# Kernel optimization log

Measured on AMD Instinct MI355X. Metric: run time of the kernel, lower is better.

The kernel has to match this reference:

```python
import jax, jax.numpy as jnp
import numpy as np
from jax import lax

DIM = 384
HEADS = 8
DS = 2  # down_scale


def setup_inputs() -> dict:
    key = jax.random.key(0)
    ks = jax.random.split(key, 6)
    d = DIM
    x = jax.random.normal(ks[0], (1, d, 192, 192), jnp.float32)
    w_qkv = jax.random.normal(ks[1], (3 * d, d), jnp.float32) * 0.02   # 1x1 conv dim->3dim
    b_qkv = jnp.zeros((3 * d,), jnp.float32)
    w_dw = jax.random.normal(ks[2], (3 * d, 1, 3, 3), jnp.float32) * 0.1  # depthwise 3x3
    b_dw = jnp.zeros((3 * d,), jnp.float32)
    w_proj = jax.random.normal(ks[3], (d, d), jnp.float32) * 0.02      # 1x1 conv dim->dim
    b_proj = jnp.zeros((d,), jnp.float32)
    temperature = jnp.ones((HEADS, 1, 1), jnp.float32)
    a1 = jnp.array([0.2], jnp.float32)
    a2 = jnp.array([0.2], jnp.float32)
    a3 = jnp.array([0.2], jnp.float32)
    a4 = jnp.array([0.2], jnp.float32)
    return {"x": x, "w_qkv": w_qkv, "b_qkv": b_qkv, "w_dw": w_dw, "b_dw": b_dw,
            "w_proj": w_proj, "b_proj": b_proj, "temperature": temperature,
            "a1": a1, "a2": a2, "a3": a3, "a4": a4}


def _topk_softmax(attn, kk):
    # exact scatter semantics of torch: mask=1 at top-k indices along last dim
    idx = lax.top_k(attn, kk)[1]                                   # [b,h,C,kk]
    mask = jax.nn.one_hot(idx, attn.shape[-1], dtype=attn.dtype).sum(-2)  # [b,h,C,C]
    return jax.nn.softmax(jnp.where(mask > 0, attn, -jnp.inf), axis=-1)


def reference(x, w_qkv, b_qkv, w_dw, b_dw, w_proj, b_proj, temperature, a1, a2, a3, a4):
    b, c, h, w = x.shape
    # 1x1 qkv conv
    qkv = jnp.einsum('bchw,oc->bohw', x, w_qkv) + b_qkv[None, :, None, None]
    # adaptive_max_pool2d to (h//DS, w//DS) == strided max pool since h,w % DS == 0
    hs, ws = h // DS, w // DS
    qkv = qkv.reshape(b, 3 * c, hs, DS, ws, DS).max(axis=(3, 5))
    # 3x3 depthwise conv, padding=1
    qkv = lax.conv_general_dilated(qkv, w_dw, (1, 1), 'SAME',
                                   feature_group_count=3 * c,
                                   dimension_numbers=('NCHW', 'OIHW', 'NCHW'))
    qkv = qkv + b_dw[None, :, None, None]
    q, k, v = jnp.split(qkv, 3, axis=1)
    hw = hs * ws
    C = c // HEADS
    q = q.reshape(b, HEADS, C, hw)
    k = k.reshape(b, HEADS, C, hw)
    v = v.reshape(b, HEADS, C, hw)
    # L2 normalize along spatial dim (F.normalize, eps=1e-12)
    q = q / jnp.clip(jnp.linalg.norm(q, axis=-1, keepdims=True), 1e-12)
    k = k / jnp.clip(jnp.linalg.norm(k, axis=-1, keepdims=True), 1e-12)
    # channel attention: [b,h,C,C]
    attn = jnp.einsum('bhcn,bhdn->bhcd', q, k) * temperature[None]
    out = (_topk_softmax(attn, C // 2) @ v) * a1 \
        + (_topk_softmax(attn, C * 2 // 3) @ v) * a2 \
        + (_topk_softmax(attn, C * 3 // 4) @ v) * a3 \
        + (_topk_softmax(attn, C * 4 // 5) @ v) * a4
    out = out.reshape(b, c, hs, ws)
    out = jax.nn.gelu(out, approximate=False)  # nn.GELU() exact erf form
    # nearest-neighbor upsample back to (h, w) == repeat by DS (exact since h = DS*hs)
    out = jnp.repeat(jnp.repeat(out, DS, axis=2), DS, axis=3)
    out = jnp.einsum('bchw,oc->bohw', out, w_proj) + b_proj[None, :, None, None]
    return out
```

## Files before the change

### kernel.cpp

```cpp
#include <hip/hip_runtime.h>
#include <hip/hip_bf16.h>
#include <math.h>

#define NH    8
#define CPH   48
#define D     384
#define QC    1152
#define HF    192
#define WFULL 192
#define HP    96
#define WP    96
#define NP    9216
#define NF    36864

typedef __attribute__((ext_vector_type(8))) short short8;
typedef __attribute__((ext_vector_type(4))) float f32x4;

__device__ __forceinline__ float gelu_exact(float v) {
    return 0.5f * v * (1.f + erff(v * 0.70710678118654752440f));
}
__device__ __forceinline__ ushort f2bf(float v) {
    __hip_bfloat16 h = __float2bfloat16(v);
    return *reinterpret_cast<ushort*>(&h);
}
__device__ __forceinline__ float bf2f(ushort u) {
    __hip_bfloat16 h = *reinterpret_cast<__hip_bfloat16*>(&u);
    return __bfloat162float(h);
}

__global__ __launch_bounds__(256) void k_prep_w(
    const float* __restrict__ w, ushort* __restrict__ wh, ushort* __restrict__ wl, int n) {
    int i = blockIdx.x * 256 + threadIdx.x;
    if (i < n) {
        float v = w[i];
        ushort h = f2bf(v);
        wh[i] = h;
        wl[i] = f2bf(v - bf2f(h));
    }
}

__global__ __launch_bounds__(256) void k_prep(
    const float* __restrict__ wq, ushort* __restrict__ wh, ushort* __restrict__ wl,
    const float* __restrict__ x, ushort* __restrict__ xh, ushort* __restrict__ xl) {
    __shared__ float xf[64][132];
    const int tid = threadIdx.x;
    if (blockIdx.x < 1728) {
        int i = blockIdx.x * 256 + tid;
        float v = wq[i];
        ushort h = f2bf(v);
        wh[i] = h;
        wl[i] = f2bf(v - bf2f(h));
        return;
    }
    const int e  = blockIdx.x - 1728;
    const int xt = e % 288, kt = e / 288;
    const int kk = kt * 64;
    const int q0 = xt * 32;
    const int py = q0 / 96, px0 = q0 - py * 96;
    const int y0 = 2 * py, xcol0 = 2 * px0;
    const float* xb = x + (size_t)kk * NF + (size_t)y0 * WFULL + xcol0;
#pragma unroll
    for (int it = 0; it < 8; it++) {
        int li = tid + 256 * it;
        int ch = li >> 5, r = (li >> 4) & 1, c4 = (li & 15) * 4;
        float4 v = *(const float4*)&xb[(size_t)ch * NF + r * WFULL + c4];
        *(float4*)&xf[ch][r * 64 + c4] = v;
    }
    __syncthreads();
    const int row = tid >> 1, half = tid & 1;
    const int r = (row >> 1) & 1;
    const int col = (row >> 2) * 2 + (row & 1);
    const int src = r * 64 + col;
    const size_t np = (size_t)xt * 128 + row;
    ushort hbuf[32], lbuf[32];
#pragma unroll
    for (int j = 0; j < 32; j++) {
        float v = xf[half * 32 + j][src];
        ushort h = f2bf(v);
        hbuf[j] = h;
        lbuf[j] = f2bf(v - bf2f(h));
    }
    ushort* dh = xh + np * D + kk + half * 32;
    ushort* dl = xl + np * D + kk + half * 32;
#pragma unroll
    for (int j = 0; j < 4; j++) {
        *(short8*)&dh[j * 8] = *(const short8*)&hbuf[j * 8];
        *(short8*)&dl[j * 8] = *(const short8*)&lbuf[j * 8];
    }
}

__global__ __launch_bounds__(512) void k_qkv_mfma(
    const ushort* __restrict__ xh, const ushort* __restrict__ xl,
    const ushort* __restrict__ wh, const ushort* __restrict__ wl,
    const float* __restrict__ bq, float* __restrict__ pooled) {
    __shared__ ushort lds[4][4096];
    const int tid = threadIdx.x;
    const int lane = tid & 63, wid = tid >> 6;
    const int wm = wid >> 2, wn = wid & 3;

    const int d   = blockIdx.x;
    const int xcd = d & 7;
    const int idx = d >> 3;
    const int by  = xcd * 36 + idx / 9;
    const int bx  = idx % 9;
    const int n0 = bx * 128;
    const int m0 = by * 128;

    const ushort* srcs[4];
    srcs[0] = xh + (size_t)m0 * D;
    srcs[1] = xl + (size_t)m0 * D;
    srcs[2] = wh + (size_t)n0 * D;
    srcs[3] = wl + (size_t)n0 * D;

    f32x4 acc[4][2];
#pragma unroll
    for (int i = 0; i < 4; i++)
#pragma unroll
        for (int j = 0; j < 2; j++) acc[i][j] = (f32x4){0.f, 0.f, 0.f, 0.f};

    int a_off[4], b_off[2];
#pragma unroll
    for (int f = 0; f < 4; f++) {
        int ra = wm * 64 + f * 16 + (lane & 15);
        a_off[f] = ra * 64 + ((((lane >> 4) ^ ((ra >> 1) & 3)) & 3) << 4);
    }
#pragma unroll
    for (int f = 0; f < 2; f++) {
        int rb = wn * 32 + f * 16 + (lane & 15);
        b_off[f] = rb * 64 + ((((lane >> 4) ^ ((rb >> 1) & 3)) & 3) << 4);
    }

    auto STAGE = [&](int kk) {
#pragma unroll
        for (int i = 0; i < 4; i++) {
            const int row = wid * 16 + (lane >> 2);
            const int scol = (((lane & 3) ^ ((row >> 1) & 3)) & 3) << 4;
            const ushort* src = srcs[i] + (size_t)row * D + kk + (scol >> 1);
            __builtin_amdgcn_global_load_lds(
                (const __attribute__((address_space(1))) void*)src,
                (__attribute__((address_space(3))) void*)&lds[i][wid * 512],
                16, 0, 0);
        }
    };

    for (int t = 0; t < 12; ++t) {
        STAGE(t * 32);
        asm volatile("s_waitcnt vmcnt(0)" ::: "memory");
        __builtin_amdgcn_s_barrier();

        const char* bA0 = (const char*)&lds[0][0];
        const char* bA1 = (const char*)&lds[1][0];
        const char* bB0 = (const char*)&lds[2][0];
        const char* bB1 = (const char*)&lds[3][0];
        short8 A[2][4], B[2][2];
#pragma unroll
        for (int f = 0; f < 4; f++) {
            A[0][f] = *(const short8*)(bA0 + a_off[f]);
            A[1][f] = *(const short8*)(bA1 + a_off[f]);
        }
#pragma unroll
        for (int f = 0; f < 2; f++) {
            B[0][f] = *(const short8*)(bB0 + b_off[f]);
            B[1][f] = *(const short8*)(bB1 + b_off[f]);
        }
        __builtin_amdgcn_s_setprio(1);
#pragma unroll
        for (int fm = 0; fm < 4; fm++)
#pragma unroll
            for (int fn = 0; fn < 2; fn++) {
                acc[fm][fn] = __builtin_amdgcn_mfma_f32_16x16x32_bf16(A[0][fm], B[0][fn], acc[fm][fn], 0, 0, 0);
                acc[fm][fn] = __builtin_amdgcn_mfma_f32_16x16x32_bf16(A[0][fm], B[1][fn], acc[fm][fn], 0, 0, 0);
                acc[fm][fn] = __builtin_amdgcn_mfma_f32_16x16x32_bf16(A[1][fm], B[0][fn], acc[fm][fn], 0, 0, 0);
            }
        __builtin_amdgcn_s_setprio(0);
        if (t < 11) __builtin_amdgcn_s_barrier();
    }

    const int p_base = by * 32 + wm * 16 + (lane >> 4);
#pragma unroll
    for (int fn = 0; fn < 2; fn++) {
        const int o = n0 + wn * 32 + fn * 16 + (lane & 15);
        const float b = bq[o];
#pragma unroll
        for (int fm = 0; fm < 4; fm++) {
            f32x4 v = acc[fm][fn];
            float mx = fmaxf(fmaxf(v.x, v.y), fmaxf(v.z, v.w)) + b;
            pooled[(size_t)o * NP + p_base + fm * 4] = mx;
        }
    }
}

__global__ __launch_bounds__(256) void k_dwconv(
    const float* __restrict__ pooled, const float* __restrict__ wd,
    const float* __restrict__ bd, float* __restrict__ out) {
    int gid = blockIdx.x * 256 + threadIdx.x;
    int xq = gid % 24, t = gid / 24;
    int y = t % 96, ch = t / 96;
    const float* src = pooled + (size_t)ch * NP;
    const float* w = wd + ch * 9;
    const int x0 = xq * 4;
    float b = bd[ch];
    float o0 = b, o1 = b, o2 = b, o3 = b;
#pragma unroll
    for (int dy = 0; dy < 3; dy++) {
        int yy = y + dy - 1;
        if (yy < 0 || yy >= HP) continue;
        const float* r = src + yy * WP;
        float4 c = *(const float4*)&r[x0];
        float lm = (x0 > 0) ? r[x0 - 1] : 0.f;
        float rm = (x0 < 92) ? r[x0 + 4] : 0.f;
        float w0 = w[dy * 3], w1 = w[dy * 3 + 1], w2 = w[dy * 3 + 2];
        o0 += w0 * lm  + w1 * c.x + w2 * c.y;
        o1 += w0 * c.x + w1 * c.y + w2 * c.z;
        o2 += w0 * c.y + w1 * c.z + w2 * c.w;
        o3 += w0 * c.z + w1 * c.w + w2 * rm;
    }
    *(float4*)&out[(size_t)ch * NP + y * WP + x0] = make_float4(o0, o1, o2, o3);
}

__global__ __launch_bounds__(256) void k_attn_part(
    const float* __restrict__ qkv, float* __restrict__ Spart,
    float* __restrict__ qnpart, float* __restrict__ knpart) {
    __shared__ float qs[48][196], ks[48][196];
    const int tid = threadIdx.x;
    const int p = blockIdx.x, h = blockIdx.y;
    const int n0 = p * 192;
    const float* qb = qkv + (size_t)(h * CPH) * NP + n0;
    const float* kb = qkv + (size_t)(D + h * CPH) * NP + n0;
#pragma unroll
    for (int it = 0; it < 9; it++) {
        int li = tid + 256 * it;
        int row = li / 48, c4 = (li - row * 48) * 4;
        *(float4*)&qs[row][c4] = *(const float4*)&qb[(size_t)row * NP + c4];
        *(float4*)&ks[row][c4] = *(const float4*)&kb[(size_t)row * NP + c4];
    }
    __syncthreads();
    const int tr = (tid >> 4) * 3, tc = (tid & 15) * 3;
    float acc[3][3] = {};
    for (int n = 0; n < 192; n++) {
        float qv[3], kv[3];
#pragma unroll
        for (int i = 0; i < 3; i++) qv[i] = qs[tr + i][n];
#pragma unroll
        for (int j = 0; j < 3; j++) kv[j] = ks[tc + j][n];
#pragma unroll
        for (int i = 0; i < 3; i++)
#pragma unroll
            for (int j = 0; j < 3; j++) acc[i][j] += qv[i] * kv[j];
    }
    float* Sp = Spart + (size_t)(p * NH + h) * 2304;
#pragma unroll
    for (int i = 0; i < 3; i++)
#pragma unroll
        for (int j = 0; j < 3; j++)
            Sp[(tr + i) * CPH + tc + j] = acc[i][j];
    if (tid < 48) {
        float s = 0.f;
        for (int n = 0; n < 192; n++) s += qs[tid][n] * qs[tid][n];
        qnpart[(p * NH + h) * CPH + tid] = s;
    } else if (tid >= 64 && tid < 112) {
        int t2 = tid - 64;
        float s = 0.f;
        for (int n = 0; n < 192; n++) s += ks[t2][n] * ks[t2][n];
        knpart[(p * NH + h) * CPH + t2] = s;
    }
}

__global__ __launch_bounds__(256) void k_softmax(
    const float* __restrict__ Spart, const float* __restrict__ qnpart,
    const float* __restrict__ knpart, const float* __restrict__ temp,
    const float* __restrict__ a1, const float* __restrict__ a2,
    const float* __restrict__ a3, const float* __restrict__ a4,
    float* __restrict__ Wc) {
    __shared__ float rowbuf[4][64];
    int lane = threadIdx.x & 63;
    int w = threadIdx.x >> 6;
    int row = blockIdx.x * 4 + w;
    int h = row / CPH, c = row % CPH;
    float a = -INFINITY;
    if (lane < CPH) {
        float s = 0.f, q2 = 0.f, k2 = 0.f;
        for (int p = 0; p < 48; p++) {
            int base = (p * NH + h);
            s  += Spart[(size_t)base * 2304 + c * CPH + lane];
            q2 += qnpart[base * CPH + c];
            k2 += knpart[base * CPH + lane];
        }
        float nq = fmaxf(sqrtf(fmaxf(q2, 0.f)), 1e-12f);
        float nk = fmaxf(sqrtf(fmaxf(k2, 0.f)), 1e-12f);
        a = s / (nq * nk) * temp[h];
    }
    rowbuf[w][lane] = a;
    __syncthreads();
    int rank = 0;
    float m = -INFINITY;
    for (int j = 0; j < CPH; j++) {
        float vj = rowbuf[w][j];
        m = fmaxf(m, vj);
        rank += (vj > a || (vj == a && j < lane)) ? 1 : 0;
    }
    float e = (lane < CPH) ? expf(a - m) : 0.f;
    float4 p;
    p.x = (rank < 24) ? e : 0.f;
    p.y = (rank < 32) ? e : 0.f;
    p.z = (rank < 36) ? e : 0.f;
    p.w = (rank < 38) ? e : 0.f;
#pragma unroll
    for (int off = 32; off > 0; off >>= 1) {
        p.x += __shfl_xor(p.x, off);
        p.y += __shfl_xor(p.y, off);
        p.z += __shfl_xor(p.z, off);
        p.w += __shfl_xor(p.w, off);
    }
    if (lane < CPH) {
        float wv = 0.f;
        if (rank < 24) wv += a1[0] / p.x;
        if (rank < 32) wv += a2[0] / p.y;
        if (rank < 36) wv += a3[0] / p.z;
        if (rank < 38) wv += a4[0] / p.w;
        Wc[(h * CPH + c) * CPH + lane] = e * wv;
    }
}

__global__ __launch_bounds__(256) void k_av_gelu(
    const float* __restrict__ qkv, const float* __restrict__ Wc,
    ushort* __restrict__ o96h, ushort* __restrict__ o96l) {
    __shared__ float Ws[3][48][16];
    __shared__ float vs[48][256];
    const int tid = threadIdx.x;
    const int b = blockIdx.x;
    const int h = b / 36;
    const int pc = b - h * 36;
    const int px0 = pc * 256;
    for (int li = tid; li < 2304; li += 256) {
        int t3 = li / 768, r = li - t3 * 768;
        int dd = r >> 4, cc = r & 15;
        Ws[t3][dd][cc] = Wc[(h * CPH + t3 * 16 + cc) * CPH + dd];
    }
    const float* vb = qkv + (size_t)(2 * D + h * CPH) * NP + px0;
#pragma unroll
    for (int it = 0; it < 12; it++) {
        int li = tid + 256 * it;
        int dd = li >> 6, c4 = (li & 63) * 4;
        *(float4*)&vs[dd][c4] = *(const float4*)&vb[(size_t)dd * NP + c4];
    }
    __syncthreads();
    for (int t3 = 0; t3 < 3; t3++) {
        float acc[16] = {};
#pragma unroll 4
        for (int dd = 0; dd < 48; dd++) {
            float vv = vs[dd][tid];
            float4 w0 = *(const float4*)&Ws[t3][dd][0];
            float4 w1 = *(const float4*)&Ws[t3][dd][4];
            float4 w2 = *(const float4*)&Ws[t3][dd][8];
            float4 w3 = *(const float4*)&Ws[t3][dd][12];
            acc[0]  += w0.x * vv; acc[1]  += w0.y * vv; acc[2]  += w0.z * vv; acc[3]  += w0.w * vv;
            acc[4]  += w1.x * vv; acc[5]  += w1.y * vv; acc[6]  += w1.z * vv; acc[7]  += w1.w * vv;
            acc[8]  += w2.x * vv; acc[9]  += w2.y * vv; acc[10] += w2.z * vv; acc[11] += w2.w * vv;
            acc[12] += w3.x * vv; acc[13] += w3.y * vv; acc[14] += w3.z * vv; acc[15] += w3.w * vv;
        }
        short8 hv0, hv1, lv0, lv1;
#pragma unroll
        for (int j = 0; j < 8; j++) {
            float g = gelu_exact(acc[j]);
            ushort hu = f2bf(g);
            hv0[j] = (short)hu; lv0[j] = (short)f2bf(g - bf2f(hu));
            float g2 = gelu_exact(acc[8 + j]);
            ushort hu2 = f2bf(g2);
            hv1[j] = (short)hu2; lv1[j] = (short)f2bf(g2 - bf2f(hu2));
        }
        size_t base = (size_t)(px0 + tid) * D + h * CPH + t3 * 16;
        *(short8*)&o96h[base] = hv0;
        *(short8*)&o96h[base + 8] = hv1;
        *(short8*)&o96l[base] = lv0;
        *(short8*)&o96l[base + 8] = lv1;
    }
}

__global__ __launch_bounds__(256) void k_proj_mfma(
    const ushort* __restrict__ wph, const ushort* __restrict__ wpl,
    const ushort* __restrict__ o96h, const ushort* __restrict__ o96l,
    const float* __restrict__ bp, float* __restrict__ out) {
    __shared__ ushort lds[2][4][4096];
    const int tid = threadIdx.x;
    const int lane = tid & 63, wid = tid >> 6;
    const int wm = wid >> 1, wn = wid & 1;

    const int d   = blockIdx.x;
    const int xcd = d & 7;
    const int idx = d >> 3;
    const int nt  = xcd * 9 + idx / 3;
    const int ot  = idx % 3;
    const int o0 = ot * 128;
    const int n0 = nt * 128;

    const ushort* srcs[4];
    srcs[0] = wph + (size_t)o0 * D;
    srcs[1] = wpl + (size_t)o0 * D;
    srcs[2] = o96h + (size_t)n0 * D;
    srcs[3] = o96l + (size_t)n0 * D;

    f32x4 acc[4][4];
#pragma unroll
    for (int i = 0; i < 4; i++)
#pragma unroll
        for (int j = 0; j < 4; j++) acc[i][j] = (f32x4){0.f, 0.f, 0.f, 0.f};

    int a_off[4], b_off[4];
#pragma unroll
    for (int f = 0; f < 4; f++) {
        int ra = wm * 64 + f * 16 + (lane & 15);
        a_off[f] = ra * 64 + ((((lane >> 4) ^ ((ra >> 1) & 3)) & 3) << 4);
        int rb = wn * 64 + f * 16 + (lane & 15);
        b_off[f] = rb * 64 + ((((lane >> 4) ^ ((rb >> 1) & 3)) & 3) << 4);
    }

    auto STAGE = [&](int buf, int kk) {
#pragma unroll
        for (int i = 0; i < 8; i++) {
            const int mat = i >> 1;
            const int cm  = ((i & 1) << 2) | wid;
            const int row = cm * 16 + (lane >> 2);
            const int scol = (((lane & 3) ^ ((row >> 1) & 3)) & 3) << 4;
            const ushort* src = srcs[mat] + (size_t)row * D + kk + (scol >> 1);
            __builtin_amdgcn_global_load_lds(
                (const __attribute__((address_space(1))) void*)src,
                (__attribute__((address_space(3))) void*)&lds[buf][mat][cm * 512],
                16, 0, 0);
        }
    };

    STAGE(0, 0);
    for (int t = 0; t < 12; ++t) {
        const int cur = t & 1;
        asm volatile("s_waitcnt vmcnt(0)" ::: "memory");
        __builtin_amdgcn_s_barrier();
        if (t < 11) STAGE(cur ^ 1, (t + 1) * 32);

        const char* bA0 = (const char*)&lds[cur][0][0];
        const char* bA1 = (const char*)&lds[cur][1][0];
        const char* bB0 = (const char*)&lds[cur][2][0];
        const char* bB1 = (const char*)&lds[cur][3][0];
        short8 A[2][4], B[2][4];
#pragma unroll
        for (int f = 0; f < 4; f++) {
            A[0][f] = *(const short8*)(bA0 + a_off[f]);
            A[1][f] = *(const short8*)(bA1 + a_off[f]);
            B[0][f] = *(const short8*)(bB0 + b_off[f]);
            B[1][f] = *(const short8*)(bB1 + b_off[f]);
        }
        __builtin_amdgcn_s_setprio(1);
#pragma unroll
        for (int fm = 0; fm < 4; fm++)
#pragma unroll
            for (int fn = 0; fn < 4; fn++) {
                acc[fm][fn] = __builtin_amdgcn_mfma_f32_16x16x32_bf16(A[0][fm], B[0][fn], acc[fm][fn], 0, 0, 0);
                acc[fm][fn] = __builtin_amdgcn_mfma_f32_16x16x32_bf16(A[0][fm], B[1][fn], acc[fm][fn], 0, 0, 0);
                acc[fm][fn] = __builtin_amdgcn_mfma_f32_16x16x32_bf16(A[1][fm], B[0][fn], acc[fm][fn], 0, 0, 0);
            }
        __builtin_amdgcn_s_setprio(0);
    }

#pragma unroll
    for (int fn = 0; fn < 4; fn++) {
        const int n = n0 + wn * 64 + fn * 16 + (lane & 15);
        const int y = n / WP, xcol = n - y * WP;
        const size_t pbase = (size_t)(2 * y) * WFULL + 2 * xcol;
#pragma unroll
        for (int fm = 0; fm < 4; fm++) {
            f32x4 v = acc[fm][fn];
#pragma unroll
            for (int j = 0; j < 4; j++) {
                const int o = o0 + wm * 64 + fm * 16 + (lane >> 4) * 4 + j;
                const float val = v[j] + bp[o];
                float2 vv = make_float2(val, val);
                size_t base = (size_t)o * NF + pbase;
                *(float2*)&out[base] = vv;
                *(float2*)&out[base + WFULL] = vv;
            }
        }
    }
}

extern "C" void kernel_launch(void* const* d_in, const int* in_sizes, int n_in,
                              void* d_out, int out_size, void* d_ws, size_t ws_size,
                              hipStream_t stream) {
    (void)in_sizes; (void)n_in; (void)out_size; (void)ws_size;
    const float* x    = (const float*)d_in[0];
    const float* wq   = (const float*)d_in[1];
    const float* bq   = (const float*)d_in[2];
    const float* wd   = (const float*)d_in[3];
    const float* bd   = (const float*)d_in[4];
    const float* wp   = (const float*)d_in[5];
    const float* bp   = (const float*)d_in[6];
    const float* temp = (const float*)d_in[7];
    const float* a1   = (const float*)d_in[8];
    const float* a2   = (const float*)d_in[9];
    const float* a3   = (const float*)d_in[10];
    const float* a4   = (const float*)d_in[11];
    float* out = (float*)d_out;
    float* ws  = (float*)d_ws;

    float* pooled = ws;
    float* Wc     = ws + 10616832;
    ushort* wh    = (ushort*)(Wc + 18432 + 19200);
    ushort* wl    = wh + 442368;

    ushort* o96h   = (ushort*)ws;
    ushort* o96l   = o96h + 3538944;
    float*  Spart  = (float*)((char*)ws + 14155776);
    float*  qnpart = Spart + 884736;
    float*  knpart = qnpart + 18432;
    ushort* wph    = (ushort*)(knpart + 18432);
    ushort* wpl    = wph + 147456;

    float* qkvdw = out;
    ushort* xh = (ushort*)d_out;
    ushort* xl = xh + 14155776;

    hipLaunchKernelGGL(k_prep,      dim3(3456),    dim3(256), 0, stream, wq, wh, wl, x, xh, xl);
    hipLaunchKernelGGL(k_qkv_mfma,  dim3(2592),    dim3(512), 0, stream, xh, xl, wh, wl, bq, pooled);
    hipLaunchKernelGGL(k_dwconv,    dim3(10368),   dim3(256), 0, stream, pooled, wd, bd, qkvdw);
    hipLaunchKernelGGL(k_prep_w,    dim3(576),     dim3(256), 0, stream, wp, wph, wpl, D * D);
    hipLaunchKernelGGL(k_attn_part, dim3(48, 8),   dim3(256), 0, stream, qkvdw, Spart, qnpart, knpart);
    hipLaunchKernelGGL(k_softmax,   dim3(96),      dim3(256), 0, stream, Spart, qnpart, knpart, temp, a1, a2, a3, a4, Wc);
    hipLaunchKernelGGL(k_av_gelu,   dim3(288),     dim3(256), 0, stream, qkvdw, Wc, o96h, o96l);
    hipLaunchKernelGGL(k_proj_mfma, dim3(216),     dim3(256), 0, stream, wph, wpl, o96h, o96l, bp, out);
}
```

Before: 231.6 us.

## Double-buffer QKV GEMM LDS staging and fold proj-weight prep into attention kernel

The QKV MFMA GEMM now uses two LDS buffers. The next K-slice is prefetched via global_load_lds while the current slice is multiplied, and one barrier per iteration is dropped. This is meant to hide global-load latency that was previously exposed on every K step, at the cost of doubling LDS use per block, which may reduce occupancy. Separately, the projection-weight bf16 split is merged into k_attn_part as extra blocks, removing one kernel launch.

```diff
diff --git a/kernel.cpp b/kernel.cpp
--- a/kernel.cpp
+++ b/kernel.cpp
@@ -26,17 +26,6 @@
 __device__ __forceinline__ float bf2f(ushort u) {
     __hip_bfloat16 h = *reinterpret_cast<__hip_bfloat16*>(&u);
     return __bfloat162float(h);
-}
-
-__global__ __launch_bounds__(256) void k_prep_w(
-    const float* __restrict__ w, ushort* __restrict__ wh, ushort* __restrict__ wl, int n) {
-    int i = blockIdx.x * 256 + threadIdx.x;
-    if (i < n) {
-        float v = w[i];
-        ushort h = f2bf(v);
-        wh[i] = h;
-        wl[i] = f2bf(v - bf2f(h));
-    }
 }
 
 __global__ __launch_bounds__(256) void k_prep(
@@ -93,7 +82,7 @@
     const ushort* __restrict__ xh, const ushort* __restrict__ xl,
     const ushort* __restrict__ wh, const ushort* __restrict__ wl,
     const float* __restrict__ bq, float* __restrict__ pooled) {
-    __shared__ ushort lds[4][4096];
+    __shared__ ushort lds[2][4][4096];
     const int tid = threadIdx.x;
     const int lane = tid & 63, wid = tid >> 6;
     const int wm = wid >> 2, wn = wid & 3;
@@ -130,7 +119,7 @@
         b_off[f] = rb * 64 + ((((lane >> 4) ^ ((rb >> 1) & 3)) & 3) << 4);
     }
 
-    auto STAGE = [&](int kk) {
+    auto STAGE = [&](int buf, int kk) {
 #pragma unroll
         for (int i = 0; i < 4; i++) {
             const int row = wid * 16 + (lane >> 2);
@@ -138,20 +127,22 @@
             const ushort* src = srcs[i] + (size_t)row * D + kk + (scol >> 1);
             __builtin_amdgcn_global_load_lds(
                 (const __attribute__((address_space(1))) void*)src,
-                (__attribute__((address_space(3))) void*)&lds[i][wid * 512],
+                (__attribute__((address_space(3))) void*)&lds[buf][i][wid * 512],
                 16, 0, 0);
         }
     };
 
+    STAGE(0, 0);
     for (int t = 0; t < 12; ++t) {
-        STAGE(t * 32);
+        const int cur = t & 1;
         asm volatile("s_waitcnt vmcnt(0)" ::: "memory");
         __builtin_amdgcn_s_barrier();
-
-        const char* bA0 = (const char*)&lds[0][0];
-        const char* bA1 = (const char*)&lds[1][0];
-        const char* bB0 = (const char*)&lds[2][0];
-        const char* bB1 = (const char*)&lds[3][0];
+        if (t < 11) STAGE(cur ^ 1, (t + 1) * 32);
+
+        const char* bA0 = (const char*)&lds[cur][0][0];
+        const char* bA1 = (const char*)&lds[cur][1][0];
+        const char* bB0 = (const char*)&lds[cur][2][0];
+        const char* bB1 = (const char*)&lds[cur][3][0];
         short8 A[2][4], B[2][2];
 #pragma unroll
         for (int f = 0; f < 4; f++) {
@@ -173,7 +164,6 @@
                 acc[fm][fn] = __builtin_amdgcn_mfma_f32_16x16x32_bf16(A[1][fm], B[0][fn], acc[fm][fn], 0, 0, 0);
             }
         __builtin_amdgcn_s_setprio(0);
-        if (t < 11) __builtin_amdgcn_s_barrier();
     }
 
     const int p_base = by * 32 + wm * 16 + (lane >> 4);
@@ -220,10 +210,19 @@
 
 __global__ __launch_bounds__(256) void k_attn_part(
     const float* __restrict__ qkv, float* __restrict__ Spart,
-    float* __restrict__ qnpart, float* __restrict__ knpart) {
+    float* __restrict__ qnpart, float* __restrict__ knpart,
+    const float* __restrict__ wp, ushort* __restrict__ wph, ushort* __restrict__ wpl) {
     __shared__ float qs[48][196], ks[48][196];
     const int tid = threadIdx.x;
-    const int p = blockIdx.x, h = blockIdx.y;
+    if (blockIdx.x >= 384) {
+        int i = (blockIdx.x - 384) * 256 + tid;
+        float v = wp[i];
+        ushort h = f2bf(v);
+        wph[i] = h;
+        wpl[i] = f2bf(v - bf2f(h));
+        return;
+    }
+    const int p = blockIdx.x >> 3, h = blockIdx.x & 7;
     const int n0 = p * 192;
     const float* qb = qkv + (size_t)(h * CPH) * NP + n0;
     const float* kb = qkv + (size_t)(D + h * CPH) * NP + n0;
@@ -521,8 +520,7 @@
     hipLaunchKernelGGL(k_prep,      dim3(3456),    dim3(256), 0, stream, wq, wh, wl, x, xh, xl);
     hipLaunchKernelGGL(k_qkv_mfma,  dim3(2592),    dim3(512), 0, stream, xh, xl, wh, wl, bq, pooled);
     hipLaunchKernelGGL(k_dwconv,    dim3(10368),   dim3(256), 0, stream, pooled, wd, bd, qkvdw);
-    hipLaunchKernelGGL(k_prep_w,    dim3(576),     dim3(256), 0, stream, wp, wph, wpl, D * D);
-    hipLaunchKernelGGL(k_attn_part, dim3(48, 8),   dim3(256), 0, stream, qkvdw, Spart, qnpart, knpart);
+    hipLaunchKernelGGL(k_attn_part, dim3(960),     dim3(256), 0, stream, qkvdw, Spart, qnpart, knpart, wp, wph, wpl);
     hipLaunchKernelGGL(k_softmax,   dim3(96),      dim3(256), 0, stream, Spart, qnpart, knpart, temp, a1, a2, a3, a4, Wc);
     hipLaunchKernelGGL(k_av_gelu,   dim3(288),     dim3(256), 0, stream, qkvdw, Wc, o96h, o96l);
     hipLaunchKernelGGL(k_proj_mfma, dim3(216),     dim3(256), 0, stream, wph, wpl, o96h, o96l, bp, out);
```

Result: faster. 215.2 us, median of 2 (-7.1%).
